# Kernel optimization log

Hardware: AMD Instinct MI355X
Metric: run time of the kernel (lower is better)

## Reference

```python
import jax, jax.numpy as jnp
import numpy as np

TEMPERATURE = 8.0  # sqrt(d_head=64)
MASK_FILL = -1e9


def setup_inputs() -> dict:
    key = jax.random.key(0)
    kq, kk, kv, km = jax.random.split(key, 4)
    B, H, L, D = 4, 16, 2048, 64
    return {
        "query": jax.random.normal(kq, (B, H, L, D), dtype=jnp.float32),
        "key": jax.random.normal(kk, (B, H, L, D), dtype=jnp.float32),
        "value": jax.random.normal(kv, (B, H, L, D), dtype=jnp.float32),
        "mask": jax.random.randint(km, (B, 1, L, L), 0, 2, dtype=jnp.int32),
    }


def reference(query, key, value, mask):
    # scores: [B, H, Lq, Lk]
    scores = jnp.einsum("bhqd,bhkd->bhqk", query / TEMPERATURE, key)
    scores = jnp.where(mask == 0, MASK_FILL, scores)
    # sigmoid attention (no row normalization); dropout omitted (eval mode)
    attn = jax.nn.sigmoid(scores)
    output = jnp.einsum("bhqk,bhkd->bhqd", attn, value)
    return (output, attn)
```

## Files before the change

### kernel.cpp

```cpp
#include <hip/hip_runtime.h>
#include <hip/hip_bf16.h>
#include <stdint.h>

#define B_ 4
#define H_ 16
#define L_ 2048
#define D_ 64
#define BH (B_ * H_)

typedef __attribute__((ext_vector_type(8))) short short8;
typedef __attribute__((ext_vector_type(4))) float f32x4;

__device__ __forceinline__ short b16(float f) {
  __hip_bfloat16 h = __float2bfloat16(f);
  return __builtin_bit_cast(short, h);
}
__device__ __forceinline__ unsigned int pkbf16(float lo, float hi) {
  return (unsigned int)(unsigned short)b16(lo) |
         ((unsigned int)(unsigned short)b16(hi) << 16);
}

__global__ __launch_bounds__(256) void vt_kernel(const float* __restrict__ V,
                                                 unsigned short* __restrict__ Vt) {
  __shared__ unsigned short lds[64 * 68];
  int bid = blockIdx.x;
  int bh  = bid >> 5;
  int kt  = bid & 31;
  int t   = threadIdx.x;
  const float* vsrc = V + ((size_t)bh * L_ + (size_t)kt * 64) * D_;
#pragma unroll
  for (int i = 0; i < 4; ++i) {
    int f4  = i * 256 + t;
    int row = f4 >> 4;
    int c4  = (f4 & 15) << 2;
    float4 v = *reinterpret_cast<const float4*>(vsrc + row * D_ + c4);
    ushort4 u;
    u.x = (unsigned short)b16(v.x);
    u.y = (unsigned short)b16(v.y);
    u.z = (unsigned short)b16(v.z);
    u.w = (unsigned short)b16(v.w);
    *reinterpret_cast<ushort4*>(&lds[row * 68 + c4]) = u;
  }
  __syncthreads();
  unsigned short* dst = Vt + (size_t)bh * D_ * L_ + (size_t)kt * 64;
#pragma unroll
  for (int i = 0; i < 8; ++i) {
    int c  = i * 256 + t;
    int d  = c >> 5;
    int k2 = (c & 31) * 2;
    unsigned int lo = lds[(k2 + 0) * 68 + d];
    unsigned int hi = lds[(k2 + 1) * 68 + d];
    *reinterpret_cast<unsigned int*>(dst + d * L_ + k2) = lo | (hi << 16);
  }
}

__global__ __launch_bounds__(256, 4) void attn6_kernel(
    const float* __restrict__ Q, const float* __restrict__ K,
    const int* __restrict__ M, const unsigned short* __restrict__ Vt,
    float* __restrict__ O, float* __restrict__ A) {
  __shared__ unsigned short Kl[2][4096];
  __shared__ unsigned short Vl[2][4096];

  int wg  = blockIdx.x;
  int xcd = wg & 7;
  int j   = wg >> 3;
  int g   = xcd * 16 + (j & 15);
  int b   = g >> 5;
  int qt  = g & 31;
  int h   = j >> 4;
  int bh  = b * 16 + h;

  int t    = threadIdx.x;
  int lane = t & 63;
  int w    = t >> 6;
  int lr   = lane & 15;
  int lg   = lane >> 4;
  int qrow0 = qt * 64 + w * 16;

  short8 qf[2];
  {
    const float* qb = Q + ((size_t)bh * L_ + qrow0 + lr) * D_;
#pragma unroll
    for (int ks = 0; ks < 2; ++ks) {
      const float4* p = reinterpret_cast<const float4*>(qb + ks * 32 + lg * 8);
      float4 a = p[0], c = p[1];
      qf[ks] = (short8){b16(a.x * 0.125f), b16(a.y * 0.125f), b16(a.z * 0.125f), b16(a.w * 0.125f),
                        b16(c.x * 0.125f), b16(c.y * 0.125f), b16(c.z * 0.125f), b16(c.w * 0.125f)};
    }
  }

  f32x4 o[4] = {};
  const int* mbase = M + (size_t)b * L_ * L_;
  float* abase = A + (size_t)bh * L_ * L_;
  const float* kbase0 = K + (size_t)bh * L_ * D_;
  const unsigned short* vbase0 = Vt + (size_t)bh * D_ * L_;

  int krow[4], kc4[4];
#pragma unroll
  for (int i = 0; i < 4; ++i) {
    int f4  = i * 256 + t;
    krow[i] = f4 >> 4;
    kc4[i]  = (f4 & 15) << 2;
  }
  int vrow[2], vc0[2];
#pragma unroll
  for (int i = 0; i < 2; ++i) {
    int gi  = i * 256 + t;
    vrow[i] = gi >> 3;
    vc0[i]  = (gi & 7) << 3;
  }

  int srcA = (lr + 16 * (2 * (lane >> 4 & 1))) << 2;
  int srcB = srcA + 64;
  bool hin = (lg & 2) != 0;

  float4 kreg[4];
  uint4  vreg[2];

#pragma unroll
  for (int i = 0; i < 4; ++i)
    kreg[i] = *reinterpret_cast<const float4*>(kbase0 + krow[i] * D_ + kc4[i]);
#pragma unroll
  for (int i = 0; i < 2; ++i)
    vreg[i] = *reinterpret_cast<const uint4*>(vbase0 + (size_t)vrow[i] * L_ + vc0[i]);
#pragma unroll
  for (int i = 0; i < 4; ++i) {
    ushort4 u;
    u.x = (unsigned short)b16(kreg[i].x);
    u.y = (unsigned short)b16(kreg[i].y);
    u.z = (unsigned short)b16(kreg[i].z);
    u.w = (unsigned short)b16(kreg[i].w);
    *reinterpret_cast<ushort4*>(&Kl[0][krow[i] * 64 + (kc4[i] ^ ((krow[i] & 7) << 3))]) = u;
  }
#pragma unroll
  for (int i = 0; i < 2; ++i)
    *reinterpret_cast<uint4*>(&Vl[0][vrow[i] * 64 + (vc0[i] ^ ((vrow[i] & 7) << 3))]) = vreg[i];
  __syncthreads();

  for (int ki = 0; ki < 32; ++ki) {
    int cur = ki & 1;
    int k0  = ki * 64;

    int4 mv[4];
#pragma unroll
    for (int n = 0; n < 4; ++n)
      mv[n] = *reinterpret_cast<const int4*>(
          mbase + (size_t)(qrow0 + lr) * L_ + k0 + n * 16 + lg * 4);

    if (ki + 1 < 32) {
      const float* ksrc = kbase0 + (size_t)(k0 + 64) * D_;
      const unsigned short* vsrc = vbase0 + k0 + 64;
#pragma unroll
      for (int i = 0; i < 4; ++i)
        kreg[i] = *reinterpret_cast<const float4*>(ksrc + krow[i] * D_ + kc4[i]);
#pragma unroll
      for (int i = 0; i < 2; ++i)
        vreg[i] = *reinterpret_cast<const uint4*>(vsrc + (size_t)vrow[i] * L_ + vc0[i]);
    }

    f32x4 s[4] = {};
#pragma unroll
    for (int ks = 0; ks < 2; ++ks) {
#pragma unroll
      for (int n = 0; n < 4; ++n) {
        int row = n * 16 + lr;
        int col = ks * 32 + lg * 8;
        short8 kf = *reinterpret_cast<const short8*>(&Kl[cur][row * 64 + (col ^ ((row & 7) << 3))]);
        s[n] = __builtin_amdgcn_mfma_f32_16x16x32_bf16(kf, qf[ks], s[n], 0, 0, 0);
      }
    }

    unsigned int c[4][2];
#pragma unroll
    for (int n = 0; n < 4; ++n) {
      f32x4 f;
#pragma unroll
      for (int r = 0; r < 4; ++r) {
        float sv = s[n][r];
        float e  = __builtin_amdgcn_exp2f(sv * -1.44269504f);
        float at = ((&mv[n].x)[r] != 0) ? __builtin_amdgcn_rcpf(1.0f + e) : 0.0f;
        f[r] = at;
      }
      __builtin_nontemporal_store(f, reinterpret_cast<f32x4*>(
          abase + (size_t)(qrow0 + lr) * L_ + k0 + n * 16 + lg * 4));
      c[n][0] = pkbf16(f[0], f[1]);
      c[n][1] = pkbf16(f[2], f[3]);
    }

    short8 pf[2];
#pragma unroll
    for (int ks = 0; ks < 2; ++ks) {
      unsigned int wv[4];
#pragma unroll
      for (int i = 0; i < 4; ++i) {
        int idx = (i >> 1) ? srcB : srcA;
        int lo = __builtin_amdgcn_ds_bpermute(idx, (int)c[2 * ks][i & 1]);
        int hi = __builtin_amdgcn_ds_bpermute(idx, (int)c[2 * ks + 1][i & 1]);
        wv[i] = (unsigned int)(hin ? hi : lo);
      }
      uint4 u4 = {wv[0], wv[1], wv[2], wv[3]};
      pf[ks] = __builtin_bit_cast(short8, u4);
    }

#pragma unroll
    for (int ks = 0; ks < 2; ++ks) {
#pragma unroll
      for (int n2 = 0; n2 < 4; ++n2) {
        int row = n2 * 16 + lr;
        int col = ks * 32 + lg * 8;
        short8 vf = *reinterpret_cast<const short8*>(&Vl[cur][row * 64 + (col ^ ((row & 7) << 3))]);
        o[n2] = __builtin_amdgcn_mfma_f32_16x16x32_bf16(pf[ks], vf, o[n2], 0, 0, 0);
      }
    }

    if (ki + 1 < 32) {
#pragma unroll
      for (int i = 0; i < 4; ++i) {
        ushort4 u;
        u.x = (unsigned short)b16(kreg[i].x);
        u.y = (unsigned short)b16(kreg[i].y);
        u.z = (unsigned short)b16(kreg[i].z);
        u.w = (unsigned short)b16(kreg[i].w);
        *reinterpret_cast<ushort4*>(&Kl[cur ^ 1][krow[i] * 64 + (kc4[i] ^ ((krow[i] & 7) << 3))]) = u;
      }
#pragma unroll
      for (int i = 0; i < 2; ++i)
        *reinterpret_cast<uint4*>(&Vl[cur ^ 1][vrow[i] * 64 + (vc0[i] ^ ((vrow[i] & 7) << 3))]) = vreg[i];
    }
    __syncthreads();
  }

  float* obase = O + ((size_t)bh * L_ + qrow0) * D_;
#pragma unroll
  for (int n2 = 0; n2 < 4; ++n2)
#pragma unroll
    for (int r = 0; r < 4; ++r)
      __builtin_nontemporal_store(o[n2][r],
          &obase[(lg * 4 + r) * D_ + n2 * 16 + lr]);
}

extern "C" void kernel_launch(void* const* d_in, const int* in_sizes, int n_in,
                              void* d_out, int out_size, void* d_ws, size_t ws_size,
                              hipStream_t stream) {
  (void)in_sizes; (void)n_in; (void)out_size; (void)ws_size;
  const float* Q = (const float*)d_in[0];
  const float* K = (const float*)d_in[1];
  const float* V = (const float*)d_in[2];
  const int*   M = (const int*)d_in[3];
  float* O = (float*)d_out;
  float* A = (float*)d_out + (size_t)BH * L_ * D_;
  unsigned short* Vt = (unsigned short*)d_ws;

  vt_kernel<<<BH * 32, 256, 0, stream>>>(V, Vt);
  attn6_kernel<<<BH * 32, 256, 0, stream>>>(Q, K, M, Vt, O, A);
}
```

Measured before the change: 318.9 us.

## Pre-convert K to bf16 and process two heads per workgroup

The prep kernel now also converts K to bf16 in workspace, alongside the transposed bf16 V. The attention kernel no longer loads fp32 K and converts it inside the main loop. Each 512-thread workgroup now covers two heads for the same query tile, so both heads read the shared per-batch mask rows close together in time and get better cache reuse. The cost is an extra prep pass over K, more LDS per block, and larger workgroups that may lower occupancy, while the kernel stays dominated by the large attention-matrix writes.

```diff
diff --git a/kernel.cpp b/kernel.cpp
--- a/kernel.cpp
+++ b/kernel.cpp
@@ -7,6 +7,7 @@
 #define L_ 2048
 #define D_ 64
 #define BH (B_ * H_)
+#define NT (BH * 32)
 
 typedef __attribute__((ext_vector_type(8))) short short8;
 typedef __attribute__((ext_vector_type(4))) float f32x4;
@@ -20,46 +21,65 @@
          ((unsigned int)(unsigned short)b16(hi) << 16);
 }
 
-__global__ __launch_bounds__(256) void vt_kernel(const float* __restrict__ V,
-                                                 unsigned short* __restrict__ Vt) {
+__global__ __launch_bounds__(256) void prep_kernel(const float* __restrict__ K,
+                                                   const float* __restrict__ V,
+                                                   unsigned short* __restrict__ Kt,
+                                                   unsigned short* __restrict__ Vt) {
   __shared__ unsigned short lds[64 * 68];
   int bid = blockIdx.x;
-  int bh  = bid >> 5;
-  int kt  = bid & 31;
   int t   = threadIdx.x;
-  const float* vsrc = V + ((size_t)bh * L_ + (size_t)kt * 64) * D_;
-#pragma unroll
-  for (int i = 0; i < 4; ++i) {
-    int f4  = i * 256 + t;
-    int row = f4 >> 4;
-    int c4  = (f4 & 15) << 2;
-    float4 v = *reinterpret_cast<const float4*>(vsrc + row * D_ + c4);
-    ushort4 u;
-    u.x = (unsigned short)b16(v.x);
-    u.y = (unsigned short)b16(v.y);
-    u.z = (unsigned short)b16(v.z);
-    u.w = (unsigned short)b16(v.w);
-    *reinterpret_cast<ushort4*>(&lds[row * 68 + c4]) = u;
-  }
-  __syncthreads();
-  unsigned short* dst = Vt + (size_t)bh * D_ * L_ + (size_t)kt * 64;
-#pragma unroll
-  for (int i = 0; i < 8; ++i) {
-    int c  = i * 256 + t;
-    int d  = c >> 5;
-    int k2 = (c & 31) * 2;
-    unsigned int lo = lds[(k2 + 0) * 68 + d];
-    unsigned int hi = lds[(k2 + 1) * 68 + d];
-    *reinterpret_cast<unsigned int*>(dst + d * L_ + k2) = lo | (hi << 16);
-  }
-}
-
-__global__ __launch_bounds__(256, 4) void attn6_kernel(
-    const float* __restrict__ Q, const float* __restrict__ K,
-    const int* __restrict__ M, const unsigned short* __restrict__ Vt,
+  if (bid < NT) {
+    const float* src = K + (size_t)bid * 64 * D_;
+    unsigned short* dst = Kt + (size_t)bid * 64 * D_;
+#pragma unroll
+    for (int i = 0; i < 4; ++i) {
+      int f4 = i * 256 + t;
+      float4 v = *reinterpret_cast<const float4*>(src + f4 * 4);
+      ushort4 u;
+      u.x = (unsigned short)b16(v.x);
+      u.y = (unsigned short)b16(v.y);
+      u.z = (unsigned short)b16(v.z);
+      u.w = (unsigned short)b16(v.w);
+      *reinterpret_cast<ushort4*>(dst + f4 * 4) = u;
+    }
+  } else {
+    bid -= NT;
+    int bh = bid >> 5;
+    int kt = bid & 31;
+    const float* vsrc = V + ((size_t)bh * L_ + (size_t)kt * 64) * D_;
+#pragma unroll
+    for (int i = 0; i < 4; ++i) {
+      int f4  = i * 256 + t;
+      int row = f4 >> 4;
+      int c4  = (f4 & 15) << 2;
+      float4 v = *reinterpret_cast<const float4*>(vsrc + row * D_ + c4);
+      ushort4 u;
+      u.x = (unsigned short)b16(v.x);
+      u.y = (unsigned short)b16(v.y);
+      u.z = (unsigned short)b16(v.z);
+      u.w = (unsigned short)b16(v.w);
+      *reinterpret_cast<ushort4*>(&lds[row * 68 + c4]) = u;
+    }
+    __syncthreads();
+    unsigned short* dst = Vt + (size_t)bh * D_ * L_ + (size_t)kt * 64;
+#pragma unroll
+    for (int i = 0; i < 8; ++i) {
+      int c  = i * 256 + t;
+      int d  = c >> 5;
+      int k2 = (c & 31) * 2;
+      unsigned int lo = lds[(k2 + 0) * 68 + d];
+      unsigned int hi = lds[(k2 + 1) * 68 + d];
+      *reinterpret_cast<unsigned int*>(dst + d * L_ + k2) = lo | (hi << 16);
+    }
+  }
+}
+
+__global__ __launch_bounds__(512, 4) void attn7_kernel(
+    const float* __restrict__ Q, const int* __restrict__ M,
+    const unsigned short* __restrict__ Kt, const unsigned short* __restrict__ Vt,
     float* __restrict__ O, float* __restrict__ A) {
-  __shared__ unsigned short Kl[2][4096];
-  __shared__ unsigned short Vl[2][4096];
+  __shared__ unsigned short Kl[2][2][4096];
+  __shared__ unsigned short Vl[2][2][4096];
 
   int wg  = blockIdx.x;
   int xcd = wg & 7;
@@ -67,15 +87,18 @@
   int g   = xcd * 16 + (j & 15);
   int b   = g >> 5;
   int qt  = g & 31;
-  int h   = j >> 4;
-  int bh  = b * 16 + h;
+  int hp  = j >> 4;
+  int bh0 = b * 16 + hp * 2;
 
   int t    = threadIdx.x;
   int lane = t & 63;
   int w    = t >> 6;
+  int head = w >> 2;
+  int strip = w & 3;
   int lr   = lane & 15;
   int lg   = lane >> 4;
-  int qrow0 = qt * 64 + w * 16;
+  int qrow0 = qt * 64 + strip * 16;
+  int bh   = bh0 + head;
 
   short8 qf[2];
   {
@@ -92,49 +115,35 @@
   f32x4 o[4] = {};
   const int* mbase = M + (size_t)b * L_ * L_;
   float* abase = A + (size_t)bh * L_ * L_;
-  const float* kbase0 = K + (size_t)bh * L_ * D_;
-  const unsigned short* vbase0 = Vt + (size_t)bh * D_ * L_;
-
-  int krow[4], kc4[4];
-#pragma unroll
-  for (int i = 0; i < 4; ++i) {
-    int f4  = i * 256 + t;
-    krow[i] = f4 >> 4;
-    kc4[i]  = (f4 & 15) << 2;
-  }
-  int vrow[2], vc0[2];
+
+  int th = t & 255, hd = t >> 8;
+  int srow[2], sc0[2];
 #pragma unroll
   for (int i = 0; i < 2; ++i) {
-    int gi  = i * 256 + t;
-    vrow[i] = gi >> 3;
-    vc0[i]  = (gi & 7) << 3;
-  }
-
-  int srcA = (lr + 16 * (2 * (lane >> 4 & 1))) << 2;
+    int g2  = i * 256 + th;
+    srow[i] = g2 >> 3;
+    sc0[i]  = (g2 & 7) << 3;
+  }
+  const unsigned short* ktb = Kt + (size_t)(bh0 + hd) * L_ * D_;
+  const unsigned short* vtb = Vt + (size_t)(bh0 + hd) * D_ * L_;
+
+  int srcA = (lr + 16 * (2 * (lg & 1))) << 2;
   int srcB = srcA + 64;
   bool hin = (lg & 2) != 0;
 
-  float4 kreg[4];
-  uint4  vreg[2];
-
-#pragma unroll
-  for (int i = 0; i < 4; ++i)
-    kreg[i] = *reinterpret_cast<const float4*>(kbase0 + krow[i] * D_ + kc4[i]);
-#pragma unroll
-  for (int i = 0; i < 2; ++i)
-    vreg[i] = *reinterpret_cast<const uint4*>(vbase0 + (size_t)vrow[i] * L_ + vc0[i]);
-#pragma unroll
-  for (int i = 0; i < 4; ++i) {
-    ushort4 u;
-    u.x = (unsigned short)b16(kreg[i].x);
-    u.y = (unsigned short)b16(kreg[i].y);
-    u.z = (unsigned short)b16(kreg[i].z);
-    u.w = (unsigned short)b16(kreg[i].w);
-    *reinterpret_cast<ushort4*>(&Kl[0][krow[i] * 64 + (kc4[i] ^ ((krow[i] & 7) << 3))]) = u;
-  }
-#pragma unroll
-  for (int i = 0; i < 2; ++i)
-    *reinterpret_cast<uint4*>(&Vl[0][vrow[i] * 64 + (vc0[i] ^ ((vrow[i] & 7) << 3))]) = vreg[i];
+  uint4 kpre[2], vpre[2];
+
+#pragma unroll
+  for (int i = 0; i < 2; ++i) {
+    kpre[i] = *reinterpret_cast<const uint4*>(ktb + (size_t)srow[i] * D_ + sc0[i]);
+    vpre[i] = *reinterpret_cast<const uint4*>(vtb + (size_t)srow[i] * L_ + sc0[i]);
+  }
+#pragma unroll
+  for (int i = 0; i < 2; ++i) {
+    int sw = sc0[i] ^ ((srow[i] & 7) << 3);
+    *reinterpret_cast<uint4*>(&Kl[hd][0][srow[i] * 64 + sw]) = kpre[i];
+    *reinterpret_cast<uint4*>(&Vl[hd][0][srow[i] * 64 + sw]) = vpre[i];
+  }
   __syncthreads();
 
   for (int ki = 0; ki < 32; ++ki) {
@@ -148,14 +157,11 @@
           mbase + (size_t)(qrow0 + lr) * L_ + k0 + n * 16 + lg * 4);
 
     if (ki + 1 < 32) {
-      const float* ksrc = kbase0 + (size_t)(k0 + 64) * D_;
-      const unsigned short* vsrc = vbase0 + k0 + 64;
-#pragma unroll
-      for (int i = 0; i < 4; ++i)
-        kreg[i] = *reinterpret_cast<const float4*>(ksrc + krow[i] * D_ + kc4[i]);
-#pragma unroll
-      for (int i = 0; i < 2; ++i)
-        vreg[i] = *reinterpret_cast<const uint4*>(vsrc + (size_t)vrow[i] * L_ + vc0[i]);
+#pragma unroll
+      for (int i = 0; i < 2; ++i) {
+        kpre[i] = *reinterpret_cast<const uint4*>(ktb + (size_t)(k0 + 64 + srow[i]) * D_ + sc0[i]);
+        vpre[i] = *reinterpret_cast<const uint4*>(vtb + (size_t)srow[i] * L_ + k0 + 64 + sc0[i]);
+      }
     }
 
     f32x4 s[4] = {};
@@ -165,7 +171,8 @@
       for (int n = 0; n < 4; ++n) {
         int row = n * 16 + lr;
         int col = ks * 32 + lg * 8;
-        short8 kf = *reinterpret_cast<const short8*>(&Kl[cur][row * 64 + (col ^ ((row & 7) << 3))]);
+        short8 kf = *reinterpret_cast<const short8*>(
+            &Kl[head][cur][row * 64 + (col ^ ((row & 7) << 3))]);
         s[n] = __builtin_amdgcn_mfma_f32_16x16x32_bf16(kf, qf[ks], s[n], 0, 0, 0);
       }
     }
@@ -208,24 +215,19 @@
       for (int n2 = 0; n2 < 4; ++n2) {
         int row = n2 * 16 + lr;
         int col = ks * 32 + lg * 8;
-        short8 vf = *reinterpret_cast<const short8*>(&Vl[cur][row * 64 + (col ^ ((row & 7) << 3))]);
+        short8 vf = *reinterpret_cast<const short8*>(
+            &Vl[head][cur][row * 64 + (col ^ ((row & 7) << 3))]);
         o[n2] = __builtin_amdgcn_mfma_f32_16x16x32_bf16(pf[ks], vf, o[n2], 0, 0, 0);
       }
     }
 
     if (ki + 1 < 32) {
 #pragma unroll
-      for (int i = 0; i < 4; ++i) {
-        ushort4 u;
-        u.x = (unsigned short)b16(kreg[i].x);
-        u.y = (unsigned short)b16(kreg[i].y);
-        u.z = (unsigned short)b16(kreg[i].z);
-        u.w = (unsigned short)b16(kreg[i].w);
-        *reinterpret_cast<ushort4*>(&Kl[cur ^ 1][krow[i] * 64 + (kc4[i] ^ ((krow[i] & 7) << 3))]) = u;
-      }
-#pragma unroll
-      for (int i = 0; i < 2; ++i)
-        *reinterpret_cast<uint4*>(&Vl[cur ^ 1][vrow[i] * 64 + (vc0[i] ^ ((vrow[i] & 7) << 3))]) = vreg[i];
+      for (int i = 0; i < 2; ++i) {
+        int sw = sc0[i] ^ ((srow[i] & 7) << 3);
+        *reinterpret_cast<uint4*>(&Kl[hd][cur ^ 1][srow[i] * 64 + sw]) = kpre[i];
+        *reinterpret_cast<uint4*>(&Vl[hd][cur ^ 1][srow[i] * 64 + sw]) = vpre[i];
+      }
     }
     __syncthreads();
   }
@@ -249,8 +251,9 @@
   const int*   M = (const int*)d_in[3];
   float* O = (float*)d_out;
   float* A = (float*)d_out + (size_t)BH * L_ * D_;
-  unsigned short* Vt = (unsigned short*)d_ws;
-
-  vt_kernel<<<BH * 32, 256, 0, stream>>>(V, Vt);
-  attn6_kernel<<<BH * 32, 256, 0, stream>>>(Q, K, M, Vt, O, A);
-}
+  unsigned short* Kt = (unsigned short*)d_ws;
+  unsigned short* Vt = (unsigned short*)d_ws + (size_t)NT * 4096;
+
+  prep_kernel<<<2 * NT, 256, 0, stream>>>(K, V, Kt, Vt);
+  attn7_kernel<<<NT / 2, 512, 0, stream>>>(Q, M, Kt, Vt, O, A);
+}
```

Result: slower. 341.0 us (+6.9%).

## Pre-pack int32 mask to bytes in prep kernel and use plain stores

Applied to the files above, without the earlier changes.

Adds a pass to the preprocessing kernel that compresses the int32 mask into a byte mask in workspace. The attention kernel then reads 4 bytes instead of 16 per lane group, so the mask traffic that was re-read by all 16 heads shrinks. The attention and output stores also switch from nontemporal to regular stores. The extra pass still reads the full int32 mask once and writes the byte copy, and regular stores may pollute the cache with the large attn output.

```diff
diff --git a/kernel.cpp b/kernel.cpp
--- a/kernel.cpp
+++ b/kernel.cpp
@@ -7,6 +7,8 @@
 #define L_ 2048
 #define D_ 64
 #define BH (B_ * H_)
+#define NT (BH * 32)
+#define MB_ 2048
 
 typedef __attribute__((ext_vector_type(8))) short short8;
 typedef __attribute__((ext_vector_type(4))) float f32x4;
@@ -20,43 +22,59 @@
          ((unsigned int)(unsigned short)b16(hi) << 16);
 }
 
-__global__ __launch_bounds__(256) void vt_kernel(const float* __restrict__ V,
-                                                 unsigned short* __restrict__ Vt) {
+__global__ __launch_bounds__(256) void prep_kernel(const float* __restrict__ V,
+                                                   const int* __restrict__ M,
+                                                   unsigned short* __restrict__ Vt,
+                                                   unsigned char* __restrict__ M8) {
   __shared__ unsigned short lds[64 * 68];
   int bid = blockIdx.x;
-  int bh  = bid >> 5;
-  int kt  = bid & 31;
   int t   = threadIdx.x;
-  const float* vsrc = V + ((size_t)bh * L_ + (size_t)kt * 64) * D_;
-#pragma unroll
-  for (int i = 0; i < 4; ++i) {
-    int f4  = i * 256 + t;
-    int row = f4 >> 4;
-    int c4  = (f4 & 15) << 2;
-    float4 v = *reinterpret_cast<const float4*>(vsrc + row * D_ + c4);
-    ushort4 u;
-    u.x = (unsigned short)b16(v.x);
-    u.y = (unsigned short)b16(v.y);
-    u.z = (unsigned short)b16(v.z);
-    u.w = (unsigned short)b16(v.w);
-    *reinterpret_cast<ushort4*>(&lds[row * 68 + c4]) = u;
-  }
-  __syncthreads();
-  unsigned short* dst = Vt + (size_t)bh * D_ * L_ + (size_t)kt * 64;
-#pragma unroll
-  for (int i = 0; i < 8; ++i) {
-    int c  = i * 256 + t;
-    int d  = c >> 5;
-    int k2 = (c & 31) * 2;
-    unsigned int lo = lds[(k2 + 0) * 68 + d];
-    unsigned int hi = lds[(k2 + 1) * 68 + d];
-    *reinterpret_cast<unsigned int*>(dst + d * L_ + k2) = lo | (hi << 16);
-  }
-}
-
-__global__ __launch_bounds__(256, 4) void attn6_kernel(
+  if (bid < NT) {
+    int bh = bid >> 5;
+    int kt = bid & 31;
+    const float* vsrc = V + ((size_t)bh * L_ + (size_t)kt * 64) * D_;
+#pragma unroll
+    for (int i = 0; i < 4; ++i) {
+      int f4  = i * 256 + t;
+      int row = f4 >> 4;
+      int c4  = (f4 & 15) << 2;
+      float4 v = *reinterpret_cast<const float4*>(vsrc + row * D_ + c4);
+      ushort4 u;
+      u.x = (unsigned short)b16(v.x);
+      u.y = (unsigned short)b16(v.y);
+      u.z = (unsigned short)b16(v.z);
+      u.w = (unsigned short)b16(v.w);
+      *reinterpret_cast<ushort4*>(&lds[row * 68 + c4]) = u;
+    }
+    __syncthreads();
+    unsigned short* dst = Vt + (size_t)bh * D_ * L_ + (size_t)kt * 64;
+#pragma unroll
+    for (int i = 0; i < 8; ++i) {
+      int c  = i * 256 + t;
+      int d  = c >> 5;
+      int k2 = (c & 31) * 2;
+      unsigned int lo = lds[(k2 + 0) * 68 + d];
+      unsigned int hi = lds[(k2 + 1) * 68 + d];
+      *reinterpret_cast<unsigned int*>(dst + d * L_ + k2) = lo | (hi << 16);
+    }
+  } else {
+    int bid2 = bid - NT;
+    const int* src = M + (size_t)bid2 * 8192;
+    unsigned char* dst = M8 + (size_t)bid2 * 8192;
+#pragma unroll
+    for (int p = 0; p < 8; ++p) {
+      int idx = (p * 256 + t) * 4;
+      int4 v = *reinterpret_cast<const int4*>(src + idx);
+      unsigned int pk = (v.x ? 1u : 0u) | (v.y ? 0x100u : 0u) |
+                        (v.z ? 0x10000u : 0u) | (v.w ? 0x1000000u : 0u);
+      *reinterpret_cast<unsigned int*>(dst + idx) = pk;
+    }
+  }
+}
+
+__global__ __launch_bounds__(256, 4) void attn8_kernel(
     const float* __restrict__ Q, const float* __restrict__ K,
-    const int* __restrict__ M, const unsigned short* __restrict__ Vt,
+    const unsigned char* __restrict__ M8, const unsigned short* __restrict__ Vt,
     float* __restrict__ O, float* __restrict__ A) {
   __shared__ unsigned short Kl[2][4096];
   __shared__ unsigned short Vl[2][4096];
@@ -90,7 +108,7 @@
   }
 
   f32x4 o[4] = {};
-  const int* mbase = M + (size_t)b * L_ * L_;
+  const unsigned char* mbase = M8 + (size_t)b * L_ * L_;
   float* abase = A + (size_t)bh * L_ * L_;
   const float* kbase0 = K + (size_t)bh * L_ * D_;
   const unsigned short* vbase0 = Vt + (size_t)bh * D_ * L_;
@@ -110,7 +128,7 @@
     vc0[i]  = (gi & 7) << 3;
   }
 
-  int srcA = (lr + 16 * (2 * (lane >> 4 & 1))) << 2;
+  int srcA = (lr + 16 * (2 * (lg & 1))) << 2;
   int srcB = srcA + 64;
   bool hin = (lg & 2) != 0;
 
@@ -141,10 +159,10 @@
     int cur = ki & 1;
     int k0  = ki * 64;
 
-    int4 mv[4];
+    unsigned int mv[4];
 #pragma unroll
     for (int n = 0; n < 4; ++n)
-      mv[n] = *reinterpret_cast<const int4*>(
+      mv[n] = *reinterpret_cast<const unsigned int*>(
           mbase + (size_t)(qrow0 + lr) * L_ + k0 + n * 16 + lg * 4);
 
     if (ki + 1 < 32) {
@@ -178,11 +196,11 @@
       for (int r = 0; r < 4; ++r) {
         float sv = s[n][r];
         float e  = __builtin_amdgcn_exp2f(sv * -1.44269504f);
-        float at = ((&mv[n].x)[r] != 0) ? __builtin_amdgcn_rcpf(1.0f + e) : 0.0f;
+        float at = ((mv[n] >> (8 * r)) & 0xFFu) ? __builtin_amdgcn_rcpf(1.0f + e) : 0.0f;
         f[r] = at;
       }
-      __builtin_nontemporal_store(f, reinterpret_cast<f32x4*>(
-          abase + (size_t)(qrow0 + lr) * L_ + k0 + n * 16 + lg * 4));
+      *reinterpret_cast<f32x4*>(
+          abase + (size_t)(qrow0 + lr) * L_ + k0 + n * 16 + lg * 4) = f;
       c[n][0] = pkbf16(f[0], f[1]);
       c[n][1] = pkbf16(f[2], f[3]);
     }
@@ -235,8 +253,7 @@
   for (int n2 = 0; n2 < 4; ++n2)
 #pragma unroll
     for (int r = 0; r < 4; ++r)
-      __builtin_nontemporal_store(o[n2][r],
-          &obase[(lg * 4 + r) * D_ + n2 * 16 + lr]);
+      obase[(lg * 4 + r) * D_ + n2 * 16 + lr] = o[n2][r];
 }
 
 extern "C" void kernel_launch(void* const* d_in, const int* in_sizes, int n_in,
@@ -250,7 +267,8 @@
   float* O = (float*)d_out;
   float* A = (float*)d_out + (size_t)BH * L_ * D_;
   unsigned short* Vt = (unsigned short*)d_ws;
-
-  vt_kernel<<<BH * 32, 256, 0, stream>>>(V, Vt);
-  attn6_kernel<<<BH * 32, 256, 0, stream>>>(Q, K, M, Vt, O, A);
-}
+  unsigned char*  M8 = (unsigned char*)d_ws + (size_t)NT * 8192;
+
+  prep_kernel<<<NT + MB_, 256, 0, stream>>>(V, M, Vt, M8);
+  attn8_kernel<<<BH * 32, 256, 0, stream>>>(Q, K, M8, Vt, O, A);
+}
```

After: 533.0 us. 67.2% more time.
